# Kernel optimization log

Measured on AMD Instinct MI355X. Metric: run time of the kernel, lower is better.

## Reference

```python
import jax, jax.numpy as jnp
import numpy as np

THRESHOLD = 0.05
TOP_N = 300
NMS_THR = 0.6
POST_TOP_N = 100
MIN_SIZE = 0
N_CLASS = 81
C = N_CLASS - 1
STRIDES = (8, 16, 32, 64, 128)
IMG_H, IMG_W = 800, 1024
B = 16


def _level_hw(s):
    return (-(-IMG_H // s), -(-IMG_W // s))


def setup_inputs() -> dict:
    key = jax.random.key(0)
    inp = {}
    for li, s in enumerate(STRIDES):
        H, W = _level_hw(s)
        key, k1, k2, k3 = jax.random.split(key, 4)
        xs = (jnp.arange(W, dtype=jnp.float32) + 0.5) * s
        ys = (jnp.arange(H, dtype=jnp.float32) + 0.5) * s
        gx, gy = jnp.meshgrid(xs, ys)  # [H, W], row-major h*W+w flatten order
        inp[f"location{li}"] = jnp.stack([gx.reshape(-1), gy.reshape(-1)], -1)
        inp[f"cls{li}"] = jax.random.normal(k1, (B, C, H, W), jnp.float32)
        inp[f"box{li}"] = jax.random.uniform(k2, (B, 4, H, W), jnp.float32) * (4.0 * s)
        inp[f"ctr{li}"] = jax.random.normal(k3, (B, 1, H, W), jnp.float32)
    inp["img_h"] = IMG_H
    inp["img_w"] = IMG_W
    return inp


def _process_level(loc, cls, box, ctr, img_h, img_w):
    b, c, h, w = cls.shape
    cls = jax.nn.sigmoid(cls.transpose(0, 2, 3, 1).reshape(b, h * w, c))
    box = box.transpose(0, 2, 3, 1).reshape(b, h * w, 4)
    ctr = jax.nn.sigmoid(ctr.reshape(b, h * w))
    score = cls * ctr[:, :, None]                 # [B, HW, C]
    masked = jnp.where(cls > THRESHOLD, score, -1.0).reshape(b, -1)
    k = min(TOP_N, masked.shape[1])
    vals, idx = jax.lax.top_k(masked, k)
    if k < TOP_N:
        vals = jnp.pad(vals, ((0, 0), (0, TOP_N - k)), constant_values=-1.0)
        idx = jnp.pad(idx, ((0, 0), (0, TOP_N - k)))
    valid = vals > 0.0                            # candidates only; pads invalid
    pos = idx // c
    label = idx % c + 1
    ssel = jnp.take_along_axis(score.reshape(b, -1), idx, axis=1)  # differentiable gather
    bsel = jnp.take_along_axis(box, pos[..., None], axis=1)        # [B, TOP_N, 4]
    lsel = loc[pos]                                                # [B, TOP_N, 2]
    # decode + clip (BoxList.clip clamps to [0, size-1])
    x1 = jnp.clip(lsel[..., 0] - bsel[..., 0], 0.0, img_w - 1.0)
    y1 = jnp.clip(lsel[..., 1] - bsel[..., 1], 0.0, img_h - 1.0)
    x2 = jnp.clip(lsel[..., 0] + bsel[..., 2], 0.0, img_w - 1.0)
    y2 = jnp.clip(lsel[..., 1] + bsel[..., 3], 0.0, img_h - 1.0)
    det = jnp.stack([x1, y1, x2, y2], -1)
    # remove_small_box: xywh with remove=1
    valid = valid & ((x2 - x1 + 1.0) >= MIN_SIZE) & ((y2 - y1 + 1.0) >= MIN_SIZE)
    scores = jnp.sqrt(jnp.maximum(ssel, 1e-12))
    return det, scores, label, valid


def _pairwise_iou(b):
    area = (b[:, 2] - b[:, 0]) * (b[:, 3] - b[:, 1])
    lt = jnp.maximum(b[:, None, :2], b[None, :, :2])
    rb = jnp.minimum(b[:, None, 2:], b[None, :, 2:])
    wh = jnp.clip(rb - lt, 0.0)
    inter = wh[..., 0] * wh[..., 1]
    union = area[:, None] + area[None, :] - inter
    return inter / jnp.maximum(union, 1e-9)


def _nms_image(boxes, scores, labels, valid, offset):
    # per-class NMS via class-offset trick: boxes of different labels never overlap
    K = boxes.shape[0]
    s = jnp.where(valid, scores, -jnp.inf)
    order = jnp.argsort(-s)
    b = boxes[order]
    v = valid[order]
    lab = labels[order]
    so = s[order]
    iou = _pairwise_iou(b + (lab.astype(b.dtype) * offset)[:, None])
    ar = jnp.arange(K)

    def body(i, keep):
        sup = (iou[i] > NMS_THR) & keep[i] & (ar > i)
        return keep & ~sup

    keep = jax.lax.fori_loop(0, K, body, v)
    s2 = jnp.where(keep, so, -jnp.inf)
    _, idx2 = jax.lax.top_k(s2, POST_TOP_N)   # post_top_n selection
    fvalid = jnp.take(keep, idx2)
    fb = jnp.where(fvalid[:, None], b[idx2], 0.0)
    fs = jnp.where(fvalid, so[idx2], 0.0)
    fl = jnp.where(fvalid, lab[idx2], 0)
    return fb, fs, fl, fvalid


def _forward(locs, clss, boxs, ctrs, img_h, img_w):
    dets, scs, labs, vals = [], [], [], []
    for loc, cl, bx, ct in zip(locs, clss, boxs, ctrs):
        d, s, l, v = _process_level(loc, cl, bx, ct, float(img_h), float(img_w))
        dets.append(d); scs.append(s); labs.append(l); vals.append(v)
    det = jnp.concatenate(dets, 1)   # [B, 5*TOP_N, 4]
    sc = jnp.concatenate(scs, 1)
    lab = jnp.concatenate(labs, 1)
    val = jnp.concatenate(vals, 1)
    offset = float(max(img_h, img_w) + 1)
    fb, fs, fl, fv = jax.vmap(lambda b_, s_, l_, v_: _nms_image(b_, s_, l_, v_, offset))(det, sc, lab, val)
    out5 = jnp.concatenate([fb, fs[..., None]], -1)  # [B, POST_TOP_N, 5]
    return out5, fl, fv


def reference(location0, location1, location2, location3, location4,
              cls0, cls1, cls2, cls3, cls4,
              box0, box1, box2, box3, box4,
              ctr0, ctr1, ctr2, ctr3, ctr4,
              img_h, img_w):
    locs = [location0, location1, location2, location3, location4]
    clss = [cls0, cls1, cls2, cls3, cls4]
    boxs = [box0, box1, box2, box3, box4]
    ctrs = [ctr0, ctr1, ctr2, ctr3, ctr4]
    return _forward(locs, clss, boxs, ctrs, img_h, img_w)
```

## Files before the change

kernel.cpp:

```cpp
#include <hip/hip_runtime.h>
#include <math.h>

#define THREADS 256

constexpr int NLEV  = 5;
constexpr int NB    = 16;
constexpr int NC    = 80;
constexpr int TOPN  = 300;
constexpr int KC    = NLEV * TOPN;
constexpr int KROWS = 1536;
constexpr int WORDS = 24;
constexpr int NTRI  = WORDS * (WORDS + 1) / 2;
constexpr int POSTN = 100;
constexpr int CAP   = 4096;
constexpr int NBINS = 2048;
constexpr int NPAIR = NLEV * NB;

constexpr int HW0 = 12800, HW1 = 3200, HW2 = 800, HW3 = 208, HW4 = 56;
constexpr int CH0 = 63, CH1 = 16, CH2 = 4, CH3 = 2, CH4 = 1;
constexpr int CHUNKS = CH0 + CH1 + CH2 + CH3 + CH4;

constexpr int SCTB0 = 0;
constexpr int SCTB1 = 204800;
constexpr int SCTB2 = 256000;
constexpr int SCTB3 = 268800;
constexpr int SCTB4 = 272128;
constexpr int SCTN  = 273024;

constexpr int GPL0 = 4000, GPL1 = 1000, GPL2 = 250, GPL3 = 65, GPL4 = 18;
constexpr int GMXB0 = 0;
constexpr int GMXB1 = GMXB0 + NB * GPL0;
constexpr int GMXB2 = GMXB1 + NB * GPL1;
constexpr int GMXB3 = GMXB2 + NB * GPL2;
constexpr int GMXB4 = GMXB3 + NB * GPL3;
constexpr int GMXN  = GMXB4 + NB * GPL4;

constexpr int GLSTRIDE = 4096;
constexpr int BPP = 16;

constexpr int HF_BIG = 1024, HF_SMALL = 1;

constexpr size_t align256(size_t x) { return (x + 255) & ~(size_t)255; }
constexpr size_t OFF_HIST = 0;
constexpr size_t OFF_CNT  = OFF_HIST + (size_t)NPAIR * NBINS * 4;
constexpr size_t OFF_CAND = align256(OFF_CNT + (size_t)NPAIR * 4);
constexpr size_t OFF_CBOX = align256(OFF_CAND + (size_t)NPAIR * CAP * 8);
constexpr size_t OFF_CSC  = align256(OFF_CBOX + (size_t)NB * KC * 4 * 4);
constexpr size_t OFF_CLB  = align256(OFF_CSC  + (size_t)NB * KC * 4);
constexpr size_t OFF_SSC  = align256(OFF_CLB  + (size_t)NB * KC * 4);
constexpr size_t OFF_SLB  = align256(OFF_SSC  + (size_t)NB * KC * 4);
constexpr size_t OFF_SBOX = align256(OFF_SLB  + (size_t)NB * KC * 4);
constexpr size_t OFF_OBOX = align256(OFF_SBOX + (size_t)NB * KC * 4 * 4);
constexpr size_t OFF_M    = align256(OFF_OBOX + (size_t)NB * KC * 4 * 4);
constexpr size_t OFF_SCT  = align256(OFF_M + (size_t)NB * KROWS * WORDS * 8);
constexpr size_t OFF_GMX  = align256(OFF_SCT + (size_t)SCTN * 4);
constexpr size_t OFF_TV   = align256(OFF_GMX + (size_t)GMXN * 2);
constexpr size_t OFF_GCNT = align256(OFF_TV + (size_t)NPAIR * 4);
constexpr size_t OFF_GL   = align256(OFF_GCNT + (size_t)NPAIR * 4);

struct Cand { float s; int i; };

__device__ __forceinline__ float sigm(float x) { return 1.0f / (1.0f + expf(-x)); }

__device__ __forceinline__ float sigf(float x) {
#if __has_builtin(__builtin_amdgcn_exp2f) && __has_builtin(__builtin_amdgcn_rcpf)
    float e = __builtin_amdgcn_exp2f(__fmul_rn(x, -1.44269504088896340736f));
    return __builtin_amdgcn_rcpf(__fadd_rn(1.0f, e));
#else
    return 1.0f / (1.0f + __expf(-x));
#endif
}

__device__ __forceinline__ unsigned scoreKey(float s) {
    unsigned b = __float_as_uint(s);
    unsigned k = (b < 0x3E800000u) ? 0u : ((b - 0x3E800000u) >> 13);
    return (k > 2047u) ? 2047u : k;
}

__device__ __forceinline__ unsigned long long readlane64(unsigned long long v, int l) {
    unsigned lo = (unsigned)__builtin_amdgcn_readlane((int)(unsigned)(v & 0xffffffffull), l);
    unsigned hi = (unsigned)__builtin_amdgcn_readlane((int)(unsigned)(v >> 32), l);
    return ((unsigned long long)hi << 32) | lo;
}

__device__ void bitonicShared(float* ss, int* si, int N) {
    for (int k = 2; k <= N; k <<= 1) {
        for (int j = k >> 1; j > 0; j >>= 1) {
            __syncthreads();
            for (int i = threadIdx.x; i < N; i += blockDim.x) {
                int ixj = i ^ j;
                if (ixj > i) {
                    float s1 = ss[i], s2 = ss[ixj];
                    int a1 = si[i], a2 = si[ixj];
                    bool bef = (s1 > s2) || (s1 == s2 && a1 < a2);
                    bool up = ((i & k) == 0);
                    if (up ? !bef : bef) { ss[i] = s2; ss[ixj] = s1; si[i] = a2; si[ixj] = a1; }
                }
            }
        }
    }
    __syncthreads();
}

__global__ __launch_bounds__(THREADS) void k_init(
        const float* t0, const float* t1, const float* t2, const float* t3, const float* t4,
        float* __restrict__ sct, unsigned* __restrict__ zp, int zn) {
    int i = blockIdx.x * THREADS + threadIdx.x;
    if (i < zn) zp[i] = 0;
    if (i < SCTN) {
        float x;
        if (i < SCTB1)      x = t0[i - SCTB0];
        else if (i < SCTB2) x = t1[i - SCTB1];
        else if (i < SCTB3) x = t2[i - SCTB2];
        else if (i < SCTB4) x = t3[i - SCTB3];
        else                x = t4[i - SCTB4];
        sct[i] = sigm(x);
    }
}

template<int HW, int SCTB, int GPL, int GMXB, int HF>
__device__ __forceinline__ void histChunkV(int chunkLocal, int b,
        const float* __restrict__ cls, const float* __restrict__ sct,
        unsigned short* __restrict__ gmx, unsigned* __restrict__ h) {
    constexpr int NE = HW * NC;
    const float* cp = cls + (size_t)b * NE;
    const float* tb = sct + SCTB + b * HW;
    unsigned short* gp = gmx + GMXB + (size_t)b * GPL;
    int w = threadIdx.x >> 6, lane = threadIdx.x & 63;
    int half = lane >> 5, hlane = lane & 31;
    for (int bi = w; bi < 32; bi += 4) {
        int ebase = (chunkLocal * 32 + bi) * 512;
        if (ebase >= NE) break;
        int e = ebase + lane * 8;
        int kmax = 0;
        if (e < NE) {
            int c = e / HW; int hwb = e - c * HW;
            float4 xa = *(const float4*)(cp + e);
            float4 xb = *(const float4*)(cp + e + 4);
            float4 ta = *(const float4*)(tb + hwb);
            float4 tc = *(const float4*)(tb + hwb + 4);
            float xs[8] = {xa.x, xa.y, xa.z, xa.w, xb.x, xb.y, xb.z, xb.w};
            float ts[8] = {ta.x, ta.y, ta.z, ta.w, tc.x, tc.y, tc.z, tc.w};
            #pragma unroll
            for (int q = 0; q < 8; ++q) {
                float scls = sigf(xs[q]);
                float s = __fmul_rn(scls, ts[q]);
                unsigned key = scoreKey(s);
                if (key >= (unsigned)HF) atomicAdd(&h[key], 1u);
                kmax = max(kmax, (int)key);
            }
        }
        #pragma unroll
        for (int sh = 1; sh < 32; sh <<= 1) kmax = max(kmax, __shfl_xor(kmax, sh, 64));
        int g = (ebase >> 8) + half;
        if (hlane == 0 && g * 256 < NE) gp[g] = (unsigned short)kmax;
    }
}

__global__ __launch_bounds__(THREADS) void k_hist(
        const float* c0, const float* c1, const float* c2, const float* c3, const float* c4,
        const float* __restrict__ sct, unsigned short* __restrict__ gmx, unsigned* ghist) {
    __shared__ unsigned h[NBINS];
    for (int k = threadIdx.x; k < NBINS; k += THREADS) h[k] = 0;
    __syncthreads();
    int cx = blockIdx.x, b = blockIdx.y;
    int li;
    if (cx < CH0)                 { histChunkV<HW0,SCTB0,GPL0,GMXB0,HF_BIG>(cx, b, c0, sct, gmx, h); li = 0; }
    else if (cx < CH0+CH1)        { histChunkV<HW1,SCTB1,GPL1,GMXB1,HF_BIG>(cx-CH0, b, c1, sct, gmx, h); li = 1; }
    else if (cx < CH0+CH1+CH2)    { histChunkV<HW2,SCTB2,GPL2,GMXB2,HF_BIG>(cx-CH0-CH1, b, c2, sct, gmx, h); li = 2; }
    else if (cx < CH0+CH1+CH2+CH3){ histChunkV<HW3,SCTB3,GPL3,GMXB3,HF_SMALL>(cx-CH0-CH1-CH2, b, c3, sct, gmx, h); li = 3; }
    else                          { histChunkV<HW4,SCTB4,GPL4,GMXB4,HF_SMALL>(cx-CH0-CH1-CH2-CH3, b, c4, sct, gmx, h); li = 4; }
    __syncthreads();
    unsigned* gp = ghist + (size_t)(li * NB + b) * NBINS;
    for (int k = threadIdx.x; k < NBINS; k += THREADS) {
        unsigned v = h[k];
        if (v) atomicAdd(&gp[k], v);
    }
}

__global__ __launch_bounds__(THREADS) void k_thresh(
        const unsigned* __restrict__ ghist, const unsigned short* __restrict__ gmx,
        unsigned* __restrict__ tvs, unsigned* __restrict__ gcntP,
        unsigned short* __restrict__ glistP) {
    __shared__ unsigned seg[THREADS];
    __shared__ unsigned shTv, lofs;
    int pid = blockIdx.x;
    int li = pid >> 4, b = pid & 15;
    const unsigned* h = ghist + (size_t)pid * NBINS;
    constexpr int SB = NBINS / THREADS;
    unsigned s = 0;
    for (int k = 0; k < SB; ++k) s += h[threadIdx.x * SB + k];
    seg[threadIdx.x] = s;
    __syncthreads();
    if (threadIdx.x == 0) {
        unsigned acc = 0; unsigned TA = 0;
        int t = THREADS - 1;
        for (; t >= 0; --t) {
            if (acc + seg[t] >= (unsigned)TOPN) break;
            acc += seg[t];
        }
        if (t >= 0) {
            int lo = t * SB;
            int bin = lo + SB - 1;
            for (; bin >= lo; --bin) { acc += h[bin]; if (acc >= (unsigned)TOPN) break; }
            TA = (unsigned)max(bin, lo);
        }
        unsigned Tv = (TA >= 1) ? (TA - 1) : 0;
        shTv = Tv;
        tvs[pid] = Tv;
        lofs = 0;
    }
    __syncthreads();
    unsigned Tv = shTv;
    int GPL, GMXB;
    switch (li) {
        case 0: GPL = GPL0; GMXB = GMXB0; break;
        case 1: GPL = GPL1; GMXB = GMXB1; break;
        case 2: GPL = GPL2; GMXB = GMXB2; break;
        case 3: GPL = GPL3; GMXB = GMXB3; break;
        default: GPL = GPL4; GMXB = GMXB4; break;
    }
    const unsigned short* gp = gmx + GMXB + (size_t)b * GPL;
    unsigned short* gl = glistP + (size_t)pid * GLSTRIDE;
    for (int g0 = 0; g0 < GPL; g0 += THREADS) {
        int g = g0 + (int)threadIdx.x;
        bool ok = (g < GPL);
        if (ok && Tv) ok = ((unsigned)gp[g] + 1u >= Tv);
        unsigned long long m = __ballot(ok);
        int nW = __popcll(m);
        if (nW) {
            unsigned wb = 0;
            if ((threadIdx.x & 63) == 0) wb = atomicAdd(&lofs, (unsigned)nW);
            wb = (unsigned)__builtin_amdgcn_readfirstlane((int)wb);
            if (ok) {
                unsigned slot = wb + (unsigned)__popcll(m & ((1ull << (threadIdx.x & 63)) - 1ull));
                gl[slot] = (unsigned short)g;
            }
        }
    }
    __syncthreads();
    if (threadIdx.x == 0) gcntP[pid] = lofs;
}

constexpr int LBUF = 1024;
constexpr int GB = 8;

template<int HW, int SCTB>
__device__ __forceinline__ void collectRange(int b, int pid, unsigned Tv,
        unsigned lo, unsigned hi, const unsigned short* __restrict__ gl,
        const float* __restrict__ cls, const float* __restrict__ sct,
        Cand* __restrict__ cd, unsigned* __restrict__ cnt,
        Cand* __restrict__ lbuf, unsigned* __restrict__ lcnt) {
    constexpr int NE = HW * NC;
    const float* cp = cls + (size_t)b * NE;
    const float* tb = sct + SCTB + b * HW;
    for (unsigned base = lo; base < hi; base += GB) {
        float xv[GB], tv[GB];
        int ev[GB];
        bool okv[GB];
        #pragma unroll
        for (int q = 0; q < GB; ++q) {
            unsigned gi = base + q;
            int g = gl[(gi < hi) ? gi : (hi - 1)];
            int e = g * 256 + (int)threadIdx.x;
            bool ok = (gi < hi) && (e < NE);
            e = ok ? e : 0;
            int c = e / HW; int hw = e - c * HW;
            xv[q] = cp[e];
            tv[q] = tb[hw];
            ev[q] = e;
            okv[q] = ok;
        }
        __builtin_amdgcn_sched_barrier(0);
        #pragma unroll
        for (int q = 0; q < GB; ++q) {
            float scls = sigm(xv[q]);
            float s = __fmul_rn(scls, tv[q]);
            unsigned key = scoreKey(s);
            bool take = okv[q] && (Tv ? (key >= Tv) : (scls > 0.05f));
            if (take) {
                int e = ev[q];
                int c = e / HW; int hw = e - c * HW;
                unsigned slot = atomicAdd(lcnt, 1u);
                if (slot < (unsigned)LBUF) { lbuf[slot].s = s; lbuf[slot].i = hw * NC + c; }
                else {
                    unsigned gs = atomicAdd(&cnt[pid], 1u);
                    if (gs < (unsigned)CAP) { cd[gs].s = s; cd[gs].i = hw * NC + c; }
                }
            }
        }
    }
}

__global__ __launch_bounds__(THREADS) void k_collect(
        const float* c0, const float* c1, const float* c2, const float* c3, const float* c4,
        const float* __restrict__ sct, const unsigned* __restrict__ tvs,
        const unsigned* __restrict__ gcntP, const unsigned short* __restrict__ glistP,
        Cand* cand, unsigned* cnt) {
    __shared__ Cand lbuf[LBUF];
    __shared__ unsigned lcnt, gbase;
    if (threadIdx.x == 0) lcnt = 0;
    __syncthreads();
    int pid = blockIdx.y;
    int li = pid >> 4, b = pid & 15;
    unsigned Tv = tvs[pid];
    unsigned n = gcntP[pid];
    unsigned per = (n + BPP - 1) / BPP;
    unsigned lo = blockIdx.x * per;
    unsigned hi = min(n, lo + per);
    const unsigned short* gl = glistP + (size_t)pid * GLSTRIDE;
    Cand* cd = cand + (size_t)pid * CAP;
    if (lo < hi) {
        switch (li) {
            case 0: collectRange<HW0,SCTB0>(b, pid, Tv, lo, hi, gl, c0, sct, cd, cnt, lbuf, &lcnt); break;
            case 1: collectRange<HW1,SCTB1>(b, pid, Tv, lo, hi, gl, c1, sct, cd, cnt, lbuf, &lcnt); break;
            case 2: collectRange<HW2,SCTB2>(b, pid, Tv, lo, hi, gl, c2, sct, cd, cnt, lbuf, &lcnt); break;
            case 3: collectRange<HW3,SCTB3>(b, pid, Tv, lo, hi, gl, c3, sct, cd, cnt, lbuf, &lcnt); break;
            default: collectRange<HW4,SCTB4>(b, pid, Tv, lo, hi, gl, c4, sct, cd, cnt, lbuf, &lcnt); break;
        }
    }
    __syncthreads();
    unsigned nl = lcnt; if (nl > (unsigned)LBUF) nl = LBUF;
    if (threadIdx.x == 0) gbase = nl ? atomicAdd(&cnt[pid], nl) : 0u;
    __syncthreads();
    for (unsigned i = threadIdx.x; i < nl; i += THREADS) {
        unsigned s = gbase + i;
        if (s < (unsigned)CAP) cd[s] = lbuf[i];
    }
}

__global__ __launch_bounds__(THREADS) void k_select(
        const Cand* __restrict__ candAll, const unsigned* __restrict__ cntAll,
        const float* l0, const float* l1, const float* l2, const float* l3, const float* l4,
        const float* b0, const float* b1, const float* b2, const float* b3, const float* b4,
        float* __restrict__ cbox, float* __restrict__ csc, int* __restrict__ clb) {
    __shared__ float ss[CAP];
    __shared__ int si[CAP];
    int pid = blockIdx.x;
    int li = pid / NB, b = pid - li * NB;
    int n = (int)min(cntAll[pid], (unsigned)CAP);
    const Cand* cd = candAll + (size_t)pid * CAP;
    int N = 2; while (N < n) N <<= 1;
    for (int k = threadIdx.x; k < N; k += THREADS) {
        if (k < n) { ss[k] = cd[k].s; si[k] = cd[k].i; }
        else       { ss[k] = -INFINITY; si[k] = 0x40000000 + k; }
    }
    __syncthreads();
    bitonicShared(ss, si, N);

    const float* locp; const float* boxp; int HW;
    switch (li) {
        case 0: locp = l0; boxp = b0; HW = HW0; break;
        case 1: locp = l1; boxp = b1; HW = HW1; break;
        case 2: locp = l2; boxp = b2; HW = HW2; break;
        case 3: locp = l3; boxp = b3; HW = HW3; break;
        default: locp = l4; boxp = b4; HW = HW4; break;
    }
    for (int j = threadIdx.x; j < TOPN; j += THREADS) {
        int cidx = b * KC + li * TOPN + j;
        bool ok = (j < n);
        float s = ok ? ss[j] : -INFINITY;
        ok = ok && (s > 0.0f);
        if (ok) {
            int idx = si[j];
            int hw = idx / NC, c = idx - hw * NC;
            float lx = locp[hw * 2 + 0], ly = locp[hw * 2 + 1];
            const float* bp = boxp + (size_t)b * 4 * HW + hw;
            float bl = bp[0], bt = bp[HW], br = bp[2 * HW], bb = bp[3 * HW];
            float x1 = fminf(fmaxf(__fsub_rn(lx, bl), 0.0f), 1023.0f);
            float y1 = fminf(fmaxf(__fsub_rn(ly, bt), 0.0f),  799.0f);
            float x2 = fminf(fmaxf(__fadd_rn(lx, br), 0.0f), 1023.0f);
            float y2 = fminf(fmaxf(__fadd_rn(ly, bb), 0.0f),  799.0f);
            cbox[cidx * 4 + 0] = x1; cbox[cidx * 4 + 1] = y1;
            cbox[cidx * 4 + 2] = x2; cbox[cidx * 4 + 3] = y2;
            csc[cidx] = sqrtf(fmaxf(s, 1e-12f));
            clb[cidx] = c + 1;
        } else {
            cbox[cidx * 4 + 0] = 0.0f; cbox[cidx * 4 + 1] = 0.0f;
            cbox[cidx * 4 + 2] = 0.0f; cbox[cidx * 4 + 3] = 0.0f;
            csc[cidx] = -INFINITY;
            clb[cidx] = 0;
        }
    }
}

__global__ __launch_bounds__(THREADS) void k_merge(
        const float* __restrict__ csc, const int* __restrict__ clb, const float* __restrict__ cbox,
        float* __restrict__ ssc, int* __restrict__ slb, float* __restrict__ sbox,
        float* __restrict__ obox) {
    int li = blockIdx.x, b = blockIdx.y;
    __shared__ float ss[KC];
    for (int k = threadIdx.x; k < KC; k += THREADS) ss[k] = csc[b * KC + k];
    __syncthreads();
    for (int j = threadIdx.x; j < TOPN; j += THREADS) {
        int k = li * TOPN + j;
        float s = ss[k];
        int rank = j;
        #pragma unroll
        for (int l = 0; l < NLEV; ++l) {
            if (l == li) continue;
            const float* seg = ss + l * TOPN;
            int lo = 0, hi = TOPN;
            if (l < li) {
                while (lo < hi) { int m = (lo + hi) >> 1; if (seg[m] >= s) lo = m + 1; else hi = m; }
            } else {
                while (lo < hi) { int m = (lo + hi) >> 1; if (seg[m] >  s) lo = m + 1; else hi = m; }
            }
            rank += lo;
        }
        int src = b * KC + k, dst = b * KC + rank;
        int lab = clb[src];
        ssc[dst] = s; slb[dst] = lab;
        float off = __fmul_rn((float)lab, 1025.0f);
        float4 v = *(const float4*)&cbox[(size_t)src * 4];
        *(float4*)&sbox[(size_t)dst * 4] = v;
        float4 o;
        o.x = __fadd_rn(v.x, off); o.y = __fadd_rn(v.y, off);
        o.z = __fadd_rn(v.z, off); o.w = __fadd_rn(v.w, off);
        *(float4*)&obox[(size_t)dst * 4] = o;
    }
}

__global__ __launch_bounds__(64) void k_iou(const float* __restrict__ obox,
                                            unsigned long long* __restrict__ MT) {
    int t = blockIdx.x, b = blockIdx.y;
    int tile = 0, rem = t;
    while (rem >= WORDS - tile) { rem -= WORDS - tile; ++tile; }
    int w = tile + rem;
    int lane = threadIdx.x;
    __shared__ float4 sj[64];
    __shared__ float aj[64];
    const float4* op = (const float4*)obox + (size_t)b * KC;
    int j0 = w * 64;
    int jl = j0 + lane;
    float4 vj = op[(jl < KC) ? jl : (KC - 1)];
    sj[lane] = vj;
    aj[lane] = __fmul_rn(__fsub_rn(vj.z, vj.x), __fsub_rn(vj.w, vj.y));
    int i = tile * 64 + lane;
    float4 bi = op[(i < KC) ? i : (KC - 1)];
    float ai = __fmul_rn(__fsub_rn(bi.z, bi.x), __fsub_rn(bi.w, bi.y));
    __syncthreads();
    unsigned long long bits = 0;
    int jmax = min(64, KC - j0);
    for (int jj = 0; jj < jmax; ++jj) {
        float4 bj = sj[jj];
        float xx1 = fmaxf(bi.x, bj.x), yy1 = fmaxf(bi.y, bj.y);
        float xx2 = fminf(bi.z, bj.z), yy2 = fminf(bi.w, bj.w);
        float ww = fmaxf(__fsub_rn(xx2, xx1), 0.0f);
        float hh = fmaxf(__fsub_rn(yy2, yy1), 0.0f);
        float inter = __fmul_rn(ww, hh);
        float uni = __fsub_rn(__fadd_rn(ai, aj[jj]), inter);
        float iou = __fdiv_rn(inter, fmaxf(uni, 1e-9f));
        bool kp = ((j0 + jj) > i) && (iou > 0.6f);
        bits |= kp ? (1ull << jj) : 0ull;
    }
    if (i >= KC) bits = 0;
    MT[((size_t)b * WORDS + w) * KROWS + i] = bits;
}

__global__ __launch_bounds__(64) void k_nms(
        const unsigned long long* __restrict__ MT, const float* __restrict__ ssc,
        const int* __restrict__ slb, const float* __restrict__ sbox, float* __restrict__ out) {
    int b = blockIdx.x, lane = threadIdx.x;
    for (int k = lane; k < POSTN * 5; k += 64) out[(size_t)b * POSTN * 5 + k] = 0.0f;
    for (int k = lane; k < POSTN; k += 64) {
        out[(size_t)NB * POSTN * 5 + b * POSTN + k] = 0.0f;
        out[(size_t)NB * POSTN * 5 + NB * POSTN + b * POSTN + k] = 0.0f;
    }
    const float* sp = ssc + b * KC;
    unsigned long long validV = 0;
    for (int c = 0; c < WORDS; ++c) {
        int i = c * 64 + lane;
        bool f = (i < KC) && (sp[i] > 0.0f);
        unsigned long long m = __ballot(f);
        validV = (lane == c) ? m : validV;
    }
    unsigned long long mybit = 1ull << lane;
    unsigned long long keptV = 0;
    const unsigned long long* Mb = MT + (size_t)b * WORDS * KROWS;

    unsigned long long pv[WORDS];
    pv[0] = Mb[lane];

    int keptTotal = 0;
    for (int t = 0; t < WORDS; ++t) {
        int tn = (t + 1 < WORDS) ? (t + 1) : t;
        const unsigned long long* cp = Mb + (size_t)tn * KROWS + lane;
        unsigned long long nv[WORDS];
        #pragma unroll
        for (int c = 0; c < WORDS; ++c) {
            int cc = (c <= tn) ? c : 0;
            nv[c] = cp[(size_t)cc * 64];
        }
        __builtin_amdgcn_sched_barrier(0);

        unsigned long long D = pv[t];
        unsigned long long acc = 0;
        #pragma unroll
        for (int c = 0; c < WORDS; ++c) {
            if (c < t) {
                unsigned long long kc = readlane64(keptV, c);
                if (kc & mybit) acc |= pv[c];
            }
        }
        #pragma unroll
        for (int s = 1; s < 64; s <<= 1) acc |= __shfl_xor(acc, s, 64);

        unsigned long long validT = readlane64(validV, t);
        unsigned long long rem = acc;
        unsigned long long sup = __ballot(D != 0ull) & validT;
        unsigned long long todoS = sup;
        while (todoS) {
            int r = __builtin_ctzll(todoS);
            todoS &= todoS - 1;
            if (!((rem >> r) & 1ull)) {
                unsigned long long Dr = readlane64(D, r);
                rem |= Dr;
                todoS &= ~Dr;
            }
        }
        unsigned long long kept = validT & ~rem;
        keptV = (lane == t) ? kept : keptV;

        keptTotal += (int)__popcll(kept);
        if (keptTotal >= POSTN) break;

        #pragma unroll
        for (int c = 0; c < WORDS; ++c) pv[c] = nv[c];
    }

    int base = 0;
    for (int c = 0; c < WORDS && base < POSTN; ++c) {
        unsigned long long kw = readlane64(keptV, c);
        bool f = (kw & mybit) != 0ull;
        int rank = base + __popcll(kw & (mybit - 1ull));
        if (f && rank < POSTN) {
            int i = c * 64 + lane;
            int src = b * KC + i;
            float* o5 = out + ((size_t)b * POSTN + rank) * 5;
            o5[0] = sbox[src * 4 + 0]; o5[1] = sbox[src * 4 + 1];
            o5[2] = sbox[src * 4 + 2]; o5[3] = sbox[src * 4 + 3];
            o5[4] = ssc[src];
            out[(size_t)NB * POSTN * 5 + b * POSTN + rank] = (float)slb[src];
            out[(size_t)NB * POSTN * 5 + NB * POSTN + b * POSTN + rank] = 1.0f;
        }
        base += __popcll(kw);
    }
}

extern "C" void kernel_launch(void* const* d_in, const int* in_sizes, int n_in,
                              void* d_out, int out_size, void* d_ws, size_t ws_size,
                              hipStream_t stream) {
    const float *loc[5], *cls[5], *box[5], *ctr[5];
    for (int l = 0; l < 5; ++l) {
        loc[l] = (const float*)d_in[l * 4 + 0];
        cls[l] = (const float*)d_in[l * 4 + 1];
        box[l] = (const float*)d_in[l * 4 + 2];
        ctr[l] = (const float*)d_in[l * 4 + 3];
    }
    char* ws = (char*)d_ws;
    unsigned* hist = (unsigned*)(ws + OFF_HIST);
    unsigned* cnt  = (unsigned*)(ws + OFF_CNT);
    Cand* cand     = (Cand*)(ws + OFF_CAND);
    float* cbox    = (float*)(ws + OFF_CBOX);
    float* csc     = (float*)(ws + OFF_CSC);
    int*   clb     = (int*)(ws + OFF_CLB);
    float* ssc     = (float*)(ws + OFF_SSC);
    int*   slb     = (int*)(ws + OFF_SLB);
    float* sbox    = (float*)(ws + OFF_SBOX);
    float* obox    = (float*)(ws + OFF_OBOX);
    unsigned long long* MT = (unsigned long long*)(ws + OFF_M);
    float* sct     = (float*)(ws + OFF_SCT);
    unsigned short* gmx = (unsigned short*)(ws + OFF_GMX);
    unsigned* tvs  = (unsigned*)(ws + OFF_TV);
    unsigned* gcntP = (unsigned*)(ws + OFF_GCNT);
    unsigned short* glistP = (unsigned short*)(ws + OFF_GL);
    float* out = (float*)d_out;

    int zn = (int)(OFF_CAND / 4);
    int initBlocks = (max(zn, SCTN) + THREADS - 1) / THREADS;
    k_init<<<initBlocks, THREADS, 0, stream>>>(
        ctr[0], ctr[1], ctr[2], ctr[3], ctr[4], sct, (unsigned*)ws, zn);
    k_hist<<<dim3(CHUNKS, NB), THREADS, 0, stream>>>(
        cls[0], cls[1], cls[2], cls[3], cls[4], sct, gmx, hist);
    k_thresh<<<NPAIR, THREADS, 0, stream>>>(hist, gmx, tvs, gcntP, glistP);
    k_collect<<<dim3(BPP, NPAIR), THREADS, 0, stream>>>(
        cls[0], cls[1], cls[2], cls[3], cls[4], sct, tvs, gcntP, glistP, cand, cnt);
    k_select<<<NPAIR, THREADS, 0, stream>>>(
        cand, cnt,
        loc[0], loc[1], loc[2], loc[3], loc[4],
        box[0], box[1], box[2], box[3], box[4],
        cbox, csc, clb);
    k_merge<<<dim3(NLEV, NB), THREADS, 0, stream>>>(csc, clb, cbox, ssc, slb, sbox, obox);
    k_iou<<<dim3(NTRI, NB), 64, 0, stream>>>(obox, MT);
    k_nms<<<NB, 64, 0, stream>>>(MT, ssc, slb, sbox, out);
}
```

Before: 247.8 us.

## Fuse threshold computation into collect and compute centerness sigmoid inline

Removes the precomputed centerness sigmoid table and the separate threshold kernel. The histogram and collect kernels now read raw centerness logits and apply sigmoid inline. Each collect block redundantly computes the threshold with a parallel suffix scan and builds its own group list slice in shared memory. This saves a kernel launch and a global round trip, at the cost of redundant per-block scans and extra sigmoid work per element.

```diff
diff --git a/kernel.cpp b/kernel.cpp
--- a/kernel.cpp
+++ b/kernel.cpp
@@ -20,13 +20,6 @@
 constexpr int CH0 = 63, CH1 = 16, CH2 = 4, CH3 = 2, CH4 = 1;
 constexpr int CHUNKS = CH0 + CH1 + CH2 + CH3 + CH4;
 
-constexpr int SCTB0 = 0;
-constexpr int SCTB1 = 204800;
-constexpr int SCTB2 = 256000;
-constexpr int SCTB3 = 268800;
-constexpr int SCTB4 = 272128;
-constexpr int SCTN  = 273024;
-
 constexpr int GPL0 = 4000, GPL1 = 1000, GPL2 = 250, GPL3 = 65, GPL4 = 18;
 constexpr int GMXB0 = 0;
 constexpr int GMXB1 = GMXB0 + NB * GPL0;
@@ -35,7 +28,6 @@
 constexpr int GMXB4 = GMXB3 + NB * GPL3;
 constexpr int GMXN  = GMXB4 + NB * GPL4;
 
-constexpr int GLSTRIDE = 4096;
 constexpr int BPP = 16;
 
 constexpr int HF_BIG = 1024, HF_SMALL = 1;
@@ -52,11 +44,7 @@
 constexpr size_t OFF_SBOX = align256(OFF_SLB  + (size_t)NB * KC * 4);
 constexpr size_t OFF_OBOX = align256(OFF_SBOX + (size_t)NB * KC * 4 * 4);
 constexpr size_t OFF_M    = align256(OFF_OBOX + (size_t)NB * KC * 4 * 4);
-constexpr size_t OFF_SCT  = align256(OFF_M + (size_t)NB * KROWS * WORDS * 8);
-constexpr size_t OFF_GMX  = align256(OFF_SCT + (size_t)SCTN * 4);
-constexpr size_t OFF_TV   = align256(OFF_GMX + (size_t)GMXN * 2);
-constexpr size_t OFF_GCNT = align256(OFF_TV + (size_t)NPAIR * 4);
-constexpr size_t OFF_GL   = align256(OFF_GCNT + (size_t)NPAIR * 4);
+constexpr size_t OFF_GMX  = align256(OFF_M + (size_t)NB * KROWS * WORDS * 8);
 
 struct Cand { float s; int i; };
 
@@ -102,29 +90,18 @@
     __syncthreads();
 }
 
-__global__ __launch_bounds__(THREADS) void k_init(
-        const float* t0, const float* t1, const float* t2, const float* t3, const float* t4,
-        float* __restrict__ sct, unsigned* __restrict__ zp, int zn) {
+__global__ __launch_bounds__(THREADS) void k_zero(unsigned* __restrict__ zp, int zn) {
     int i = blockIdx.x * THREADS + threadIdx.x;
     if (i < zn) zp[i] = 0;
-    if (i < SCTN) {
-        float x;
-        if (i < SCTB1)      x = t0[i - SCTB0];
-        else if (i < SCTB2) x = t1[i - SCTB1];
-        else if (i < SCTB3) x = t2[i - SCTB2];
-        else if (i < SCTB4) x = t3[i - SCTB3];
-        else                x = t4[i - SCTB4];
-        sct[i] = sigm(x);
-    }
-}
-
-template<int HW, int SCTB, int GPL, int GMXB, int HF>
+}
+
+template<int HW, int GPL, int GMXB, int HF>
 __device__ __forceinline__ void histChunkV(int chunkLocal, int b,
-        const float* __restrict__ cls, const float* __restrict__ sct,
+        const float* __restrict__ cls, const float* __restrict__ ctr,
         unsigned short* __restrict__ gmx, unsigned* __restrict__ h) {
     constexpr int NE = HW * NC;
     const float* cp = cls + (size_t)b * NE;
-    const float* tb = sct + SCTB + b * HW;
+    const float* tb = ctr + (size_t)b * HW;
     unsigned short* gp = gmx + GMXB + (size_t)b * GPL;
     int w = threadIdx.x >> 6, lane = threadIdx.x & 63;
     int half = lane >> 5, hlane = lane & 31;
@@ -144,7 +121,7 @@
             #pragma unroll
             for (int q = 0; q < 8; ++q) {
                 float scls = sigf(xs[q]);
-                float s = __fmul_rn(scls, ts[q]);
+                float s = __fmul_rn(scls, sigf(ts[q]));
                 unsigned key = scoreKey(s);
                 if (key >= (unsigned)HF) atomicAdd(&h[key], 1u);
                 kmax = max(kmax, (int)key);
@@ -159,17 +136,18 @@
 
 __global__ __launch_bounds__(THREADS) void k_hist(
         const float* c0, const float* c1, const float* c2, const float* c3, const float* c4,
-        const float* __restrict__ sct, unsigned short* __restrict__ gmx, unsigned* ghist) {
+        const float* t0, const float* t1, const float* t2, const float* t3, const float* t4,
+        unsigned short* __restrict__ gmx, unsigned* ghist) {
     __shared__ unsigned h[NBINS];
     for (int k = threadIdx.x; k < NBINS; k += THREADS) h[k] = 0;
     __syncthreads();
     int cx = blockIdx.x, b = blockIdx.y;
     int li;
-    if (cx < CH0)                 { histChunkV<HW0,SCTB0,GPL0,GMXB0,HF_BIG>(cx, b, c0, sct, gmx, h); li = 0; }
-    else if (cx < CH0+CH1)        { histChunkV<HW1,SCTB1,GPL1,GMXB1,HF_BIG>(cx-CH0, b, c1, sct, gmx, h); li = 1; }
-    else if (cx < CH0+CH1+CH2)    { histChunkV<HW2,SCTB2,GPL2,GMXB2,HF_BIG>(cx-CH0-CH1, b, c2, sct, gmx, h); li = 2; }
-    else if (cx < CH0+CH1+CH2+CH3){ histChunkV<HW3,SCTB3,GPL3,GMXB3,HF_SMALL>(cx-CH0-CH1-CH2, b, c3, sct, gmx, h); li = 3; }
-    else                          { histChunkV<HW4,SCTB4,GPL4,GMXB4,HF_SMALL>(cx-CH0-CH1-CH2-CH3, b, c4, sct, gmx, h); li = 4; }
+    if (cx < CH0)                 { histChunkV<HW0,GPL0,GMXB0,HF_BIG>(cx, b, c0, t0, gmx, h); li = 0; }
+    else if (cx < CH0+CH1)        { histChunkV<HW1,GPL1,GMXB1,HF_BIG>(cx-CH0, b, c1, t1, gmx, h); li = 1; }
+    else if (cx < CH0+CH1+CH2)    { histChunkV<HW2,GPL2,GMXB2,HF_BIG>(cx-CH0-CH1, b, c2, t2, gmx, h); li = 2; }
+    else if (cx < CH0+CH1+CH2+CH3){ histChunkV<HW3,GPL3,GMXB3,HF_SMALL>(cx-CH0-CH1-CH2, b, c3, t3, gmx, h); li = 3; }
+    else                          { histChunkV<HW4,GPL4,GMXB4,HF_SMALL>(cx-CH0-CH1-CH2-CH3, b, c4, t4, gmx, h); li = 4; }
     __syncthreads();
     unsigned* gp = ghist + (size_t)(li * NB + b) * NBINS;
     for (int k = threadIdx.x; k < NBINS; k += THREADS) {
@@ -178,96 +156,32 @@
     }
 }
 
-__global__ __launch_bounds__(THREADS) void k_thresh(
-        const unsigned* __restrict__ ghist, const unsigned short* __restrict__ gmx,
-        unsigned* __restrict__ tvs, unsigned* __restrict__ gcntP,
-        unsigned short* __restrict__ glistP) {
-    __shared__ unsigned seg[THREADS];
-    __shared__ unsigned shTv, lofs;
-    int pid = blockIdx.x;
-    int li = pid >> 4, b = pid & 15;
-    const unsigned* h = ghist + (size_t)pid * NBINS;
-    constexpr int SB = NBINS / THREADS;
-    unsigned s = 0;
-    for (int k = 0; k < SB; ++k) s += h[threadIdx.x * SB + k];
-    seg[threadIdx.x] = s;
-    __syncthreads();
-    if (threadIdx.x == 0) {
-        unsigned acc = 0; unsigned TA = 0;
-        int t = THREADS - 1;
-        for (; t >= 0; --t) {
-            if (acc + seg[t] >= (unsigned)TOPN) break;
-            acc += seg[t];
-        }
-        if (t >= 0) {
-            int lo = t * SB;
-            int bin = lo + SB - 1;
-            for (; bin >= lo; --bin) { acc += h[bin]; if (acc >= (unsigned)TOPN) break; }
-            TA = (unsigned)max(bin, lo);
-        }
-        unsigned Tv = (TA >= 1) ? (TA - 1) : 0;
-        shTv = Tv;
-        tvs[pid] = Tv;
-        lofs = 0;
-    }
-    __syncthreads();
-    unsigned Tv = shTv;
-    int GPL, GMXB;
-    switch (li) {
-        case 0: GPL = GPL0; GMXB = GMXB0; break;
-        case 1: GPL = GPL1; GMXB = GMXB1; break;
-        case 2: GPL = GPL2; GMXB = GMXB2; break;
-        case 3: GPL = GPL3; GMXB = GMXB3; break;
-        default: GPL = GPL4; GMXB = GMXB4; break;
-    }
-    const unsigned short* gp = gmx + GMXB + (size_t)b * GPL;
-    unsigned short* gl = glistP + (size_t)pid * GLSTRIDE;
-    for (int g0 = 0; g0 < GPL; g0 += THREADS) {
-        int g = g0 + (int)threadIdx.x;
-        bool ok = (g < GPL);
-        if (ok && Tv) ok = ((unsigned)gp[g] + 1u >= Tv);
-        unsigned long long m = __ballot(ok);
-        int nW = __popcll(m);
-        if (nW) {
-            unsigned wb = 0;
-            if ((threadIdx.x & 63) == 0) wb = atomicAdd(&lofs, (unsigned)nW);
-            wb = (unsigned)__builtin_amdgcn_readfirstlane((int)wb);
-            if (ok) {
-                unsigned slot = wb + (unsigned)__popcll(m & ((1ull << (threadIdx.x & 63)) - 1ull));
-                gl[slot] = (unsigned short)g;
-            }
-        }
-    }
-    __syncthreads();
-    if (threadIdx.x == 0) gcntP[pid] = lofs;
-}
-
 constexpr int LBUF = 1024;
 constexpr int GB = 8;
 
-template<int HW, int SCTB>
-__device__ __forceinline__ void collectRange(int b, int pid, unsigned Tv,
-        unsigned lo, unsigned hi, const unsigned short* __restrict__ gl,
-        const float* __restrict__ cls, const float* __restrict__ sct,
+template<int HW>
+__device__ __forceinline__ void procList(int b, int pid, unsigned Tv, unsigned n,
+        const unsigned short* __restrict__ glist,
+        const float* __restrict__ cls, const float* __restrict__ ctr,
         Cand* __restrict__ cd, unsigned* __restrict__ cnt,
         Cand* __restrict__ lbuf, unsigned* __restrict__ lcnt) {
     constexpr int NE = HW * NC;
     const float* cp = cls + (size_t)b * NE;
-    const float* tb = sct + SCTB + b * HW;
-    for (unsigned base = lo; base < hi; base += GB) {
-        float xv[GB], tv[GB];
+    const float* tb = ctr + (size_t)b * HW;
+    for (unsigned base = 0; base < n; base += GB) {
+        float xv[GB], rv[GB];
         int ev[GB];
         bool okv[GB];
         #pragma unroll
         for (int q = 0; q < GB; ++q) {
             unsigned gi = base + q;
-            int g = gl[(gi < hi) ? gi : (hi - 1)];
+            int g = glist[(gi < n) ? gi : (n - 1)];
             int e = g * 256 + (int)threadIdx.x;
-            bool ok = (gi < hi) && (e < NE);
+            bool ok = (gi < n) && (e < NE);
             e = ok ? e : 0;
             int c = e / HW; int hw = e - c * HW;
             xv[q] = cp[e];
-            tv[q] = tb[hw];
+            rv[q] = tb[hw];
             ev[q] = e;
             okv[q] = ok;
         }
@@ -275,7 +189,7 @@
         #pragma unroll
         for (int q = 0; q < GB; ++q) {
             float scls = sigm(xv[q]);
-            float s = __fmul_rn(scls, tv[q]);
+            float s = __fmul_rn(scls, sigm(rv[q]));
             unsigned key = scoreKey(s);
             bool take = okv[q] && (Tv ? (key >= Tv) : (scls > 0.05f));
             if (take) {
@@ -294,38 +208,93 @@
 
 __global__ __launch_bounds__(THREADS) void k_collect(
         const float* c0, const float* c1, const float* c2, const float* c3, const float* c4,
-        const float* __restrict__ sct, const unsigned* __restrict__ tvs,
-        const unsigned* __restrict__ gcntP, const unsigned short* __restrict__ glistP,
+        const float* t0, const float* t1, const float* t2, const float* t3, const float* t4,
+        const unsigned* __restrict__ ghist, const unsigned short* __restrict__ gmx,
         Cand* cand, unsigned* cnt) {
+    __shared__ unsigned sfx[THREADS];
+    __shared__ int tstar;
+    __shared__ unsigned shTv;
     __shared__ Cand lbuf[LBUF];
-    __shared__ unsigned lcnt, gbase;
-    if (threadIdx.x == 0) lcnt = 0;
-    __syncthreads();
+    __shared__ unsigned lcnt, gbase, gcnt;
+    __shared__ unsigned short glist[THREADS];
+    int tid = (int)threadIdx.x;
     int pid = blockIdx.y;
     int li = pid >> 4, b = pid & 15;
-    unsigned Tv = tvs[pid];
-    unsigned n = gcntP[pid];
-    unsigned per = (n + BPP - 1) / BPP;
-    unsigned lo = blockIdx.x * per;
-    unsigned hi = min(n, lo + per);
-    const unsigned short* gl = glistP + (size_t)pid * GLSTRIDE;
+    if (tid == 0) { lcnt = 0; gcnt = 0; tstar = -1; }
+
+    const unsigned* h = ghist + (size_t)pid * NBINS;
+    unsigned s = 0;
+    #pragma unroll
+    for (int k = 0; k < 8; ++k) s += h[tid * 8 + k];
+    sfx[tid] = s;
+    for (int d = 1; d < THREADS; d <<= 1) {
+        __syncthreads();
+        unsigned v = (tid + d < THREADS) ? sfx[tid + d] : 0u;
+        __syncthreads();
+        sfx[tid] += v;
+    }
+    __syncthreads();
+    if (sfx[tid] >= (unsigned)TOPN && (tid == THREADS - 1 || sfx[tid + 1] < (unsigned)TOPN))
+        tstar = tid;
+    __syncthreads();
+    if (tid == 0) {
+        unsigned TA = 0;
+        int t = tstar;
+        if (t >= 0) {
+            unsigned acc = (t < THREADS - 1) ? sfx[t + 1] : 0u;
+            int lo = t * 8, bin = lo + 7;
+            for (; bin >= lo; --bin) { acc += h[bin]; if (acc >= (unsigned)TOPN) break; }
+            TA = (unsigned)max(bin, lo);
+        }
+        shTv = (TA >= 1) ? (TA - 1) : 0u;
+    }
+    __syncthreads();
+    unsigned Tv = shTv;
+
+    int GPL, GMXB;
+    switch (li) {
+        case 0: GPL = GPL0; GMXB = GMXB0; break;
+        case 1: GPL = GPL1; GMXB = GMXB1; break;
+        case 2: GPL = GPL2; GMXB = GMXB2; break;
+        case 3: GPL = GPL3; GMXB = GMXB3; break;
+        default: GPL = GPL4; GMXB = GMXB4; break;
+    }
+    const unsigned short* gp = gmx + GMXB + (size_t)b * GPL;
+    int per = (GPL + BPP - 1) / BPP;
+    int lo = (int)blockIdx.x * per;
+    int hi = min(GPL, lo + per);
+    {
+        int g = lo + tid;
+        bool ok = (g < hi);
+        if (ok && Tv) ok = ((unsigned)gp[g] + 1u >= Tv);
+        unsigned long long m = __ballot(ok);
+        int nW = __popcll(m);
+        if (nW) {
+            unsigned wb = 0;
+            if ((tid & 63) == 0) wb = atomicAdd(&gcnt, (unsigned)nW);
+            wb = (unsigned)__builtin_amdgcn_readfirstlane((int)wb);
+            if (ok) glist[wb + (unsigned)__popcll(m & ((1ull << (tid & 63)) - 1ull))] = (unsigned short)g;
+        }
+    }
+    __syncthreads();
+    unsigned n = gcnt;
     Cand* cd = cand + (size_t)pid * CAP;
-    if (lo < hi) {
+    if (n) {
         switch (li) {
-            case 0: collectRange<HW0,SCTB0>(b, pid, Tv, lo, hi, gl, c0, sct, cd, cnt, lbuf, &lcnt); break;
-            case 1: collectRange<HW1,SCTB1>(b, pid, Tv, lo, hi, gl, c1, sct, cd, cnt, lbuf, &lcnt); break;
-            case 2: collectRange<HW2,SCTB2>(b, pid, Tv, lo, hi, gl, c2, sct, cd, cnt, lbuf, &lcnt); break;
-            case 3: collectRange<HW3,SCTB3>(b, pid, Tv, lo, hi, gl, c3, sct, cd, cnt, lbuf, &lcnt); break;
-            default: collectRange<HW4,SCTB4>(b, pid, Tv, lo, hi, gl, c4, sct, cd, cnt, lbuf, &lcnt); break;
+            case 0: procList<HW0>(b, pid, Tv, n, glist, c0, t0, cd, cnt, lbuf, &lcnt); break;
+            case 1: procList<HW1>(b, pid, Tv, n, glist, c1, t1, cd, cnt, lbuf, &lcnt); break;
+            case 2: procList<HW2>(b, pid, Tv, n, glist, c2, t2, cd, cnt, lbuf, &lcnt); break;
+            case 3: procList<HW3>(b, pid, Tv, n, glist, c3, t3, cd, cnt, lbuf, &lcnt); break;
+            default: procList<HW4>(b, pid, Tv, n, glist, c4, t4, cd, cnt, lbuf, &lcnt); break;
         }
     }
     __syncthreads();
     unsigned nl = lcnt; if (nl > (unsigned)LBUF) nl = LBUF;
-    if (threadIdx.x == 0) gbase = nl ? atomicAdd(&cnt[pid], nl) : 0u;
-    __syncthreads();
-    for (unsigned i = threadIdx.x; i < nl; i += THREADS) {
-        unsigned s = gbase + i;
-        if (s < (unsigned)CAP) cd[s] = lbuf[i];
+    if (tid == 0) gbase = nl ? atomicAdd(&cnt[pid], nl) : 0u;
+    __syncthreads();
+    for (unsigned i = tid; i < nl; i += THREADS) {
+        unsigned sl = gbase + i;
+        if (sl < (unsigned)CAP) cd[sl] = lbuf[i];
     }
 }
 
@@ -570,22 +539,17 @@
     float* sbox    = (float*)(ws + OFF_SBOX);
     float* obox    = (float*)(ws + OFF_OBOX);
     unsigned long long* MT = (unsigned long long*)(ws + OFF_M);
-    float* sct     = (float*)(ws + OFF_SCT);
     unsigned short* gmx = (unsigned short*)(ws + OFF_GMX);
-    unsigned* tvs  = (unsigned*)(ws + OFF_TV);
-    unsigned* gcntP = (unsigned*)(ws + OFF_GCNT);
-    unsigned short* glistP = (unsigned short*)(ws + OFF_GL);
     float* out = (float*)d_out;
 
     int zn = (int)(OFF_CAND / 4);
-    int initBlocks = (max(zn, SCTN) + THREADS - 1) / THREADS;
-    k_init<<<initBlocks, THREADS, 0, stream>>>(
-        ctr[0], ctr[1], ctr[2], ctr[3], ctr[4], sct, (unsigned*)ws, zn);
+    k_zero<<<(zn + THREADS - 1) / THREADS, THREADS, 0, stream>>>((unsigned*)ws, zn);
     k_hist<<<dim3(CHUNKS, NB), THREADS, 0, stream>>>(
-        cls[0], cls[1], cls[2], cls[3], cls[4], sct, gmx, hist);
-    k_thresh<<<NPAIR, THREADS, 0, stream>>>(hist, gmx, tvs, gcntP, glistP);
+        cls[0], cls[1], cls[2], cls[3], cls[4],
+        ctr[0], ctr[1], ctr[2], ctr[3], ctr[4], gmx, hist);
     k_collect<<<dim3(BPP, NPAIR), THREADS, 0, stream>>>(
-        cls[0], cls[1], cls[2], cls[3], cls[4], sct, tvs, gcntP, glistP, cand, cnt);
+        cls[0], cls[1], cls[2], cls[3], cls[4],
+        ctr[0], ctr[1], ctr[2], ctr[3], ctr[4], hist, gmx, cand, cnt);
     k_select<<<NPAIR, THREADS, 0, stream>>>(
         cand, cnt,
         loc[0], loc[1], loc[2], loc[3], loc[4],
```

New measurement: 240.2 us. -3.1%, faster.
